# Kernel tuning notes

Hardware: AMD Instinct MI355X
Metric: run time of the kernel (lower is better)

The kernel has to match this reference:

```python
import jax, jax.numpy as jnp
import numpy as np

RADIUS = 0.2
NSAMPLE = 64


def _ball_query(xyz, new_xyz):
    """PointNet++-style ball query: first NSAMPLE point indices within RADIUS
    of each center; empty slots filled with the first found index.
    xyz: (B, N, 3), new_xyz: (B, P, 3) -> idx: (B, P, NSAMPLE) int32."""
    N = xyz.shape[1]
    # squared distances (B, P, N)
    d2 = jnp.sum((new_xyz[:, :, None, :] - xyz[:, None, :, :]) ** 2, axis=-1)
    # score = point index if inside ball else sentinel N; smallest NSAMPLE scores
    # give the first NSAMPLE in-ball indices in ascending order (CUDA order).
    scores = jnp.where(d2 < RADIUS * RADIUS, jnp.arange(N, dtype=jnp.int32), N)
    neg_vals, _ = jax.lax.top_k(-scores, NSAMPLE)
    idx = -neg_vals  # ascending smallest scores
    first = idx[..., :1]
    return jnp.where(idx < N, idx, first)


def setup_inputs() -> dict:
    key = jax.random.key(0)
    k1, k2, k3 = jax.random.split(key, 3)
    B, N, P, C = 4, 16384, 1024, 128
    xyz = jax.random.uniform(k1, (B, N, 3), dtype=jnp.float32)
    new_xyz = jax.random.uniform(k2, (B, P, 3), dtype=jnp.float32)
    features = jax.random.normal(k3, (B, C, N), dtype=jnp.float32)
    return {"xyz": xyz, "new_xyz": new_xyz, "features": features}


def reference(xyz, new_xyz, features):
    B, N, _ = xyz.shape
    idx0 = _ball_query(xyz, new_xyz)  # (B, P, S), returned as bq_idx
    # dedup: slots (other than slot 0) equal to the first index are the
    # padding fills -> redirect them to the shadow point at index N
    first = idx0[..., :1]
    dup = (idx0 == first).at[..., 0].set(False)
    idx = jnp.where(dup, N, idx0)

    # shadow xyz = 1e6, shadow feature = 0
    xyz_pad = jnp.concatenate([xyz, jnp.full((B, 1, 3), 1.0e6, xyz.dtype)], axis=1)
    grouped_xyz = jax.vmap(lambda p, i: p[i])(xyz_pad, idx)        # (B, P, S, 3)
    grouped_xyz = grouped_xyz.transpose(0, 3, 1, 2)                # (B, 3, P, S)
    grouped_xyz = grouped_xyz - new_xyz.transpose(0, 2, 1)[..., None]

    feats_pad = jnp.concatenate([features, jnp.zeros_like(features[:, :, :1])], axis=-1)
    grouped_feat = jax.vmap(lambda p, i: p[i])(feats_pad.transpose(0, 2, 1), idx)  # (B, P, S, C)
    grouped_feat = grouped_feat.transpose(0, 3, 1, 2)              # (B, C, P, S)

    # use_xyz=True: zero shadow coords, normalize by radius, concat
    xyz_feature = jnp.where(grouped_xyz > 1.0e5, 0.0, grouped_xyz) / RADIUS
    new_features = jnp.concatenate([xyz_feature, grouped_feat], axis=1)  # (B, 3+C, P, S)
    return new_features, grouped_xyz, idx0
```

## Files before the change

### kernel.cpp

```cpp
#include <hip/hip_runtime.h>
#include <cstdint>

#define BQ_B 4
#define BQ_N 16384
#define BQ_P 1024
#define BQ_C 128
#define NS   64
#define R2   0.04f

#define O1 ((size_t)BQ_B * 131 * BQ_P * NS)
#define O2 (O1 + (size_t)BQ_B * 3 * BQ_P * NS)

#define WS_T_BYTES ((size_t)BQ_B * BQ_N * BQ_C * 4)

__global__ __launch_bounds__(256) void transpose_kernel(
    const float* __restrict__ f, float* __restrict__ ft)
{
    const int bid = blockIdx.x;
    const int n0 = (bid & 255) * 64;
    const int c0 = ((bid >> 8) & 1) * 64;
    const int b  = bid >> 9;
    __shared__ float tile[64][65];

    const float* fb = f + ((size_t)b * BQ_C + c0) * BQ_N;
    #pragma unroll
    for (int k = 0; k < 16; ++k) {
        const int cc = k * 4 + (threadIdx.x >> 6);
        const int nn = threadIdx.x & 63;
        tile[cc][nn] = fb[(size_t)cc * BQ_N + n0 + nn];
    }
    __syncthreads();
    float* ob = ft + ((size_t)b * BQ_N + n0) * BQ_C + c0;
    #pragma unroll
    for (int k = 0; k < 16; ++k) {
        const int nn = k * 4 + (threadIdx.x >> 6);
        const int cc = threadIdx.x & 63;
        ob[(size_t)nn * BQ_C + cc] = tile[cc][nn];
    }
}

__global__ __launch_bounds__(256) void ballquery_kernel(
    const float* __restrict__ xyz,
    const float* __restrict__ new_xyz,
    int* __restrict__ wsIdx,
    float* __restrict__ out)
{
#pragma clang fp contract(off)
    const int center = blockIdx.x;
    const int b = center >> 10;
    const int p = center & (BQ_P - 1);
    const int t = threadIdx.x;
    const int lane = t & 63;
    const int w = t >> 6;

    __shared__ unsigned long long smask[64];
    __shared__ int sprefix[64];
    __shared__ int s_total;
    __shared__ int lds_idx[NS];

    const float cx = new_xyz[center * 3 + 0];
    const float cy = new_xyz[center * 3 + 1];
    const float cz = new_xyz[center * 3 + 2];
    const float* xb = xyz + (size_t)b * BQ_N * 3;

    int total = 0;
    const unsigned long long lmask = (1ull << lane) - 1ull;

    for (int round = 0; round < 4; ++round) {
        const int rbase = round * 4096;
        #pragma unroll
        for (int k = 0; k < 16; ++k) {
            const int j = w * 16 + k;
            const int i = rbase + j * 64 + lane;
            const float dx = xb[i * 3 + 0] - cx;
            const float dy = xb[i * 3 + 1] - cy;
            const float dz = xb[i * 3 + 2] - cz;
            const float d2 = dx * dx + dy * dy + dz * dz;
            const unsigned long long m = __ballot(d2 < R2);
            if (lane == 0) smask[j] = m;
        }
        __syncthreads();

        if (w == 0) {
            const unsigned long long mm = smask[lane];
            const int cnt = (int)__popcll(mm);
            int x = cnt;
            #pragma unroll
            for (int d = 1; d < 64; d <<= 1) {
                const int y = __shfl_up(x, d, 64);
                if (lane >= d) x += y;
            }
            sprefix[lane] = total + (x - cnt);
            if (lane == 63) s_total = total + x;
        }
        __syncthreads();

        const int new_total = s_total;
        #pragma unroll
        for (int k = 0; k < 16; ++k) {
            const int j = w * 16 + k;
            const unsigned long long m = smask[j];
            const int baser = sprefix[j];
            if (baser < NS && ((m >> lane) & 1ull)) {
                const int r = baser + (int)__popcll(m & lmask);
                if (r < NS) lds_idx[r] = rbase + j * 64 + lane;
            }
        }
        total = new_total;
        if (new_total >= NS) break;
    }
    __syncthreads();

    if (t < NS) {
        const int tt = (total > NS) ? NS : total;
        const int first = (total > 0) ? lds_idx[0] : BQ_N;
        const int v = (t < tt) ? lds_idx[t] : BQ_N;
        const int idx0 = (t < tt) ? v : first;
        const bool real = v < BQ_N;

        wsIdx[(size_t)center * NS + t] = v;
        out[O2 + (size_t)center * NS + t] = (float)idx0;

        #pragma unroll
        for (int d = 0; d < 3; ++d) {
            const float c = (d == 0) ? cx : ((d == 1) ? cy : cz);
            const float pt = real ? xb[v * 3 + d] : 1000000.0f;
            const float g = pt - c;
            out[O1 + ((size_t)(b * 3 + d) * BQ_P + p) * NS + t] = g;
            const float xf = ((g > 100000.0f) ? 0.0f : g) / 0.2f;
            out[((size_t)(b * 131 + d) * BQ_P + p) * NS + t] = xf;
        }
    }
}

__global__ __launch_bounds__(256) void row_gather_kernel(
    const float* __restrict__ ft,
    const int* __restrict__ wsIdx,
    float* __restrict__ out)
{
    const int center = blockIdx.x;
    const int b = center >> 10;
    const int p = center & (BQ_P - 1);
    const int t = threadIdx.x;

    __shared__ int   sg[NS];
    __shared__ float tile[NS][BQ_C + 1];

    if (t < NS) sg[t] = wsIdx[(size_t)center * NS + t];
    __syncthreads();

    const float* fb = ft + (size_t)b * BQ_N * BQ_C;
    #pragma unroll
    for (int k = 0; k < 8; ++k) {
        const int s  = k * 8 + (t >> 5);
        const int c4 = (t & 31) * 4;
        const int gi = sg[s];
        float4 v = make_float4(0.f, 0.f, 0.f, 0.f);
        if (gi < BQ_N) v = *(const float4*)(fb + (size_t)gi * BQ_C + c4);
        tile[s][c4 + 0] = v.x;
        tile[s][c4 + 1] = v.y;
        tile[s][c4 + 2] = v.z;
        tile[s][c4 + 3] = v.w;
    }
    __syncthreads();
    float* op = out + ((size_t)(b * 131 + 3) * BQ_P + p) * NS;
    #pragma unroll
    for (int k = 0; k < 8; ++k) {
        const int c  = k * 16 + (t >> 4);
        const int s4 = (t & 15) * 4;
        float4 v = make_float4(tile[s4 + 0][c], tile[s4 + 1][c],
                               tile[s4 + 2][c], tile[s4 + 3][c]);
        *(float4*)(op + (size_t)c * (BQ_P * NS) + s4) = v;
    }
}

extern "C" void kernel_launch(void* const* d_in, const int* in_sizes, int n_in,
                              void* d_out, int out_size, void* d_ws, size_t ws_size,
                              hipStream_t stream) {
    const float* xyz      = (const float*)d_in[0];
    const float* new_xyz  = (const float*)d_in[1];
    const float* features = (const float*)d_in[2];
    float* out = (float*)d_out;
    float* ft    = (float*)d_ws;
    int*   wsIdx = (int*)((char*)d_ws + WS_T_BYTES);

    transpose_kernel<<<dim3(BQ_B * 2 * 256), dim3(256), 0, stream>>>(features, ft);
    ballquery_kernel<<<dim3(BQ_B * BQ_P), dim3(256), 0, stream>>>(xyz, new_xyz, wsIdx, out);
    row_gather_kernel<<<dim3(BQ_B * BQ_P), dim3(256), 0, stream>>>(ft, wsIdx, out);
}
```

Measured before the change: 229.3 us.

## Drop feature transpose; gather per channel row from LDS; one wave per center

Removes the separate transpose pass. The feature gather now loads each (batch, channel) row of 16384 floats into shared memory and writes every grouped sample for that channel with coalesced float4 stores. Ball query is restructured so each wave handles one center, scanning in chunks of 512 points with ballot and popcount compaction and no block barriers, which enables early exit per center. The gather re-reads the index array once per channel and uses 64KB of LDS per block, which limits occupancy.

```diff
diff --git a/kernel.cpp b/kernel.cpp
--- a/kernel.cpp
+++ b/kernel.cpp
@@ -11,33 +11,6 @@
 #define O1 ((size_t)BQ_B * 131 * BQ_P * NS)
 #define O2 (O1 + (size_t)BQ_B * 3 * BQ_P * NS)
 
-#define WS_T_BYTES ((size_t)BQ_B * BQ_N * BQ_C * 4)
-
-__global__ __launch_bounds__(256) void transpose_kernel(
-    const float* __restrict__ f, float* __restrict__ ft)
-{
-    const int bid = blockIdx.x;
-    const int n0 = (bid & 255) * 64;
-    const int c0 = ((bid >> 8) & 1) * 64;
-    const int b  = bid >> 9;
-    __shared__ float tile[64][65];
-
-    const float* fb = f + ((size_t)b * BQ_C + c0) * BQ_N;
-    #pragma unroll
-    for (int k = 0; k < 16; ++k) {
-        const int cc = k * 4 + (threadIdx.x >> 6);
-        const int nn = threadIdx.x & 63;
-        tile[cc][nn] = fb[(size_t)cc * BQ_N + n0 + nn];
-    }
-    __syncthreads();
-    float* ob = ft + ((size_t)b * BQ_N + n0) * BQ_C + c0;
-    #pragma unroll
-    for (int k = 0; k < 16; ++k) {
-        const int nn = k * 4 + (threadIdx.x >> 6);
-        const int cc = threadIdx.x & 63;
-        ob[(size_t)nn * BQ_C + cc] = tile[cc][nn];
-    }
-}
 
 __global__ __launch_bounds__(256) void ballquery_kernel(
     const float* __restrict__ xyz,
@@ -46,131 +19,95 @@
     float* __restrict__ out)
 {
 #pragma clang fp contract(off)
-    const int center = blockIdx.x;
+    const int lane = threadIdx.x & 63;
+    const int w    = threadIdx.x >> 6;
+    const int center = blockIdx.x * 4 + w;
     const int b = center >> 10;
     const int p = center & (BQ_P - 1);
-    const int t = threadIdx.x;
-    const int lane = t & 63;
-    const int w = t >> 6;
 
-    __shared__ unsigned long long smask[64];
-    __shared__ int sprefix[64];
-    __shared__ int s_total;
-    __shared__ int lds_idx[NS];
+    __shared__ int lidx[4][NS];
 
     const float cx = new_xyz[center * 3 + 0];
     const float cy = new_xyz[center * 3 + 1];
     const float cz = new_xyz[center * 3 + 2];
     const float* xb = xyz + (size_t)b * BQ_N * 3;
 
+    const unsigned long long lmask = (1ull << lane) - 1ull;
     int total = 0;
-    const unsigned long long lmask = (1ull << lane) - 1ull;
 
-    for (int round = 0; round < 4; ++round) {
-        const int rbase = round * 4096;
+    for (int base = 0; base < BQ_N; base += 512) {
+        float d2a[8];
         #pragma unroll
-        for (int k = 0; k < 16; ++k) {
-            const int j = w * 16 + k;
-            const int i = rbase + j * 64 + lane;
+        for (int u = 0; u < 8; ++u) {
+            const int i = base + u * 64 + lane;
             const float dx = xb[i * 3 + 0] - cx;
             const float dy = xb[i * 3 + 1] - cy;
             const float dz = xb[i * 3 + 2] - cz;
-            const float d2 = dx * dx + dy * dy + dz * dz;
-            const unsigned long long m = __ballot(d2 < R2);
-            if (lane == 0) smask[j] = m;
+            d2a[u] = dx * dx + dy * dy + dz * dz;
         }
-        __syncthreads();
+        #pragma unroll
+        for (int u = 0; u < 8; ++u) {
+            const unsigned long long m = __ballot(d2a[u] < R2);
+            if ((m >> lane) & 1ull) {
+                const int r = total + (int)__popcll(m & lmask);
+                if (r < NS) lidx[w][r] = base + u * 64 + lane;
+            }
+            total += (int)__popcll(m);
+        }
+        if (total >= NS) break;
+    }
+    __threadfence_block();
 
-        if (w == 0) {
-            const unsigned long long mm = smask[lane];
-            const int cnt = (int)__popcll(mm);
-            int x = cnt;
-            #pragma unroll
-            for (int d = 1; d < 64; d <<= 1) {
-                const int y = __shfl_up(x, d, 64);
-                if (lane >= d) x += y;
-            }
-            sprefix[lane] = total + (x - cnt);
-            if (lane == 63) s_total = total + x;
-        }
-        __syncthreads();
+    const int tt    = (total > NS) ? NS : total;
+    const int first = (total > 0) ? lidx[w][0] : BQ_N;
+    const int v     = (lane < tt) ? lidx[w][lane] : BQ_N;
+    const int idx0  = (lane < tt) ? v : first;
+    const bool real = v < BQ_N;
 
-        const int new_total = s_total;
-        #pragma unroll
-        for (int k = 0; k < 16; ++k) {
-            const int j = w * 16 + k;
-            const unsigned long long m = smask[j];
-            const int baser = sprefix[j];
-            if (baser < NS && ((m >> lane) & 1ull)) {
-                const int r = baser + (int)__popcll(m & lmask);
-                if (r < NS) lds_idx[r] = rbase + j * 64 + lane;
-            }
-        }
-        total = new_total;
-        if (new_total >= NS) break;
-    }
-    __syncthreads();
+    wsIdx[(size_t)center * NS + lane] = v;
+    out[O2 + (size_t)center * NS + lane] = (float)idx0;
 
-    if (t < NS) {
-        const int tt = (total > NS) ? NS : total;
-        const int first = (total > 0) ? lds_idx[0] : BQ_N;
-        const int v = (t < tt) ? lds_idx[t] : BQ_N;
-        const int idx0 = (t < tt) ? v : first;
-        const bool real = v < BQ_N;
-
-        wsIdx[(size_t)center * NS + t] = v;
-        out[O2 + (size_t)center * NS + t] = (float)idx0;
-
-        #pragma unroll
-        for (int d = 0; d < 3; ++d) {
-            const float c = (d == 0) ? cx : ((d == 1) ? cy : cz);
-            const float pt = real ? xb[v * 3 + d] : 1000000.0f;
-            const float g = pt - c;
-            out[O1 + ((size_t)(b * 3 + d) * BQ_P + p) * NS + t] = g;
-            const float xf = ((g > 100000.0f) ? 0.0f : g) / 0.2f;
-            out[((size_t)(b * 131 + d) * BQ_P + p) * NS + t] = xf;
-        }
+    #pragma unroll
+    for (int d = 0; d < 3; ++d) {
+        const float c  = (d == 0) ? cx : ((d == 1) ? cy : cz);
+        const float pt = real ? xb[v * 3 + d] : 1000000.0f;
+        const float g  = pt - c;
+        out[O1 + ((size_t)(b * 3 + d) * BQ_P + p) * NS + lane] = g;
+        const float xf = ((g > 100000.0f) ? 0.0f : g) / 0.2f;
+        out[((size_t)(b * 131 + d) * BQ_P + p) * NS + lane] = xf;
     }
 }
 
-__global__ __launch_bounds__(256) void row_gather_kernel(
-    const float* __restrict__ ft,
+__global__ __launch_bounds__(512) void feat_gather_kernel(
+    const float* __restrict__ features,
     const int* __restrict__ wsIdx,
     float* __restrict__ out)
 {
-    const int center = blockIdx.x;
-    const int b = center >> 10;
-    const int p = center & (BQ_P - 1);
+    const int b = blockIdx.x >> 7;
+    const int c = blockIdx.x & 127;
     const int t = threadIdx.x;
 
-    __shared__ int   sg[NS];
-    __shared__ float tile[NS][BQ_C + 1];
+    __shared__ float row[BQ_N];
 
-    if (t < NS) sg[t] = wsIdx[(size_t)center * NS + t];
+    const float4* fr = (const float4*)(features + ((size_t)b * BQ_C + c) * BQ_N);
+    float4* row4 = (float4*)row;
+    #pragma unroll
+    for (int k = 0; k < 8; ++k)
+        row4[k * 512 + t] = fr[k * 512 + t];
     __syncthreads();
 
-    const float* fb = ft + (size_t)b * BQ_N * BQ_C;
-    #pragma unroll
-    for (int k = 0; k < 8; ++k) {
-        const int s  = k * 8 + (t >> 5);
-        const int c4 = (t & 31) * 4;
-        const int gi = sg[s];
-        float4 v = make_float4(0.f, 0.f, 0.f, 0.f);
-        if (gi < BQ_N) v = *(const float4*)(fb + (size_t)gi * BQ_C + c4);
-        tile[s][c4 + 0] = v.x;
-        tile[s][c4 + 1] = v.y;
-        tile[s][c4 + 2] = v.z;
-        tile[s][c4 + 3] = v.w;
-    }
-    __syncthreads();
-    float* op = out + ((size_t)(b * 131 + 3) * BQ_P + p) * NS;
-    #pragma unroll
-    for (int k = 0; k < 8; ++k) {
-        const int c  = k * 16 + (t >> 4);
-        const int s4 = (t & 15) * 4;
-        float4 v = make_float4(tile[s4 + 0][c], tile[s4 + 1][c],
-                               tile[s4 + 2][c], tile[s4 + 3][c]);
-        *(float4*)(op + (size_t)c * (BQ_P * NS) + s4) = v;
+    const int4* gi4 = (const int4*)(wsIdx + (size_t)b * BQ_P * NS);
+    float4* op = (float4*)(out + (size_t)(b * 131 + 3 + c) * BQ_P * NS);
+    #pragma unroll 4
+    for (int k = 0; k < 32; ++k) {
+        const int q = k * 512 + t;
+        const int4 gi = gi4[q];
+        float4 v;
+        v.x = (gi.x < BQ_N) ? row[gi.x] : 0.0f;
+        v.y = (gi.y < BQ_N) ? row[gi.y] : 0.0f;
+        v.z = (gi.z < BQ_N) ? row[gi.z] : 0.0f;
+        v.w = (gi.w < BQ_N) ? row[gi.w] : 0.0f;
+        op[q] = v;
     }
 }
 
@@ -181,10 +118,8 @@
     const float* new_xyz  = (const float*)d_in[1];
     const float* features = (const float*)d_in[2];
     float* out = (float*)d_out;
-    float* ft    = (float*)d_ws;
-    int*   wsIdx = (int*)((char*)d_ws + WS_T_BYTES);
+    int*   wsIdx = (int*)d_ws;
 
-    transpose_kernel<<<dim3(BQ_B * 2 * 256), dim3(256), 0, stream>>>(features, ft);
-    ballquery_kernel<<<dim3(BQ_B * BQ_P), dim3(256), 0, stream>>>(xyz, new_xyz, wsIdx, out);
-    row_gather_kernel<<<dim3(BQ_B * BQ_P), dim3(256), 0, stream>>>(ft, wsIdx, out);
+    ballquery_kernel<<<dim3(BQ_B * BQ_P / 4), dim3(256), 0, stream>>>(xyz, new_xyz, wsIdx, out);
+    feat_gather_kernel<<<dim3(BQ_B * BQ_C), dim3(512), 0, stream>>>(features, wsIdx, out);
 }
```

New measurement: 196.2 us. -14.4%, faster.
